# Performance work log

Hardware: AMD Instinct MI355X
Metric: run time of the kernel (lower is better)

The kernel has to match this reference:

```python
import jax, jax.numpy as jnp
import numpy as np

NEG_SLOPE = 0.2

def setup_inputs() -> dict:
    key = jax.random.key(0)
    ks = jax.random.split(key, 10)
    N, E, L, D, H = 100000, 3200000, 200000, 128, 128
    x = jax.random.normal(ks[0], (N, D), dtype=jnp.float32)
    edge_index = jax.random.randint(ks[1], (2, E), 0, N, dtype=jnp.int64)
    edge_label_index = jax.random.randint(ks[2], (2, L), 0, N, dtype=jnp.int64)
    s = 1.0 / np.sqrt(D)
    W1l = jax.random.uniform(ks[3], (D, H), minval=-s, maxval=s, dtype=jnp.float32)
    b1 = jax.random.uniform(ks[4], (H,), minval=-s, maxval=s, dtype=jnp.float32)
    W1r = jax.random.uniform(ks[5], (D, H), minval=-s, maxval=s, dtype=jnp.float32)
    s2 = 1.0 / np.sqrt(H)
    W2l = jax.random.uniform(ks[6], (H, H), minval=-s2, maxval=s2, dtype=jnp.float32)
    b2 = jax.random.uniform(ks[7], (H,), minval=-s2, maxval=s2, dtype=jnp.float32)
    W2r = jax.random.uniform(ks[8], (H, H), minval=-s2, maxval=s2, dtype=jnp.float32)
    return {"x": x, "edge_index": edge_index, "edge_label_index": edge_label_index,
            "W1l": W1l, "b1": b1, "W1r": W1r, "W2l": W2l, "b2": b2, "W2r": W2r}

def reference(x, edge_index, edge_label_index, W1l, b1, W1r, W2l, b2, W2r):
    N = x.shape[0]
    src, dst = edge_index[0], edge_index[1]
    # in-degree for mean aggregation (clamped to avoid div-by-zero, matching mean over empty = 0)
    deg = jax.ops.segment_sum(jnp.ones_like(dst, dtype=x.dtype), dst, num_segments=N)
    inv_deg = (1.0 / jnp.maximum(deg, 1.0))[:, None]

    def sage(h, Wl, b, Wr):
        # mean of source-node features over incoming edges at each target node
        agg = jax.ops.segment_sum(h[src], dst, num_segments=N) * inv_deg
        return agg @ Wl + b + h @ Wr

    h = sage(x, W1l, b1, W1r)
    h = jnp.where(h >= 0, h, NEG_SLOPE * h)  # leaky_relu; eval mode so no dropout
    h = sage(h, W2l, b2, W2r)
    x_src = h[edge_label_index[0]]
    x_trg = h[edge_label_index[1]]
    return jnp.sum(x_src * x_trg, axis=1)
```

## Files before the change

kernel.cpp:

```cpp
#include <hip/hip_runtime.h>
#include <hip/hip_fp16.h>


#define D128 128
#define BSHIFT 9
#define BNODES 512

typedef __bf16 bf16x8 __attribute__((ext_vector_type(8)));
typedef float  f32x4  __attribute__((ext_vector_type(4)));
typedef _Float16 h2   __attribute__((ext_vector_type(2)));

union uh2cast { unsigned u; h2 h; };
__device__ inline h2 uash2(unsigned u) { uh2cast c; c.u = u; return c.h; }

__device__ inline unsigned short f2bf(float f) {
    unsigned u = __float_as_uint(f);
    u = u + 0x7FFF + ((u >> 16) & 1);
    return (unsigned short)(u >> 16);
}
__device__ inline float bf2f(unsigned short s) {
    return __uint_as_float(((unsigned)s) << 16);
}
__device__ inline unsigned packbf2(float lo, float hi) {
    return (unsigned)f2bf(lo) | ((unsigned)f2bf(hi) << 16);
}
__device__ inline unsigned char f2e5(float f) {
    unsigned short h = __half_as_ushort(__float2half(f));
    h = (unsigned short)(h + 0x7F + ((h >> 8) & 1));
    return (unsigned char)(h >> 8);
}


__global__ void prep_kernel(const float* __restrict__ in, unsigned short* __restrict__ outb,
                            unsigned char* __restrict__ out8, int n4,
                            const float* __restrict__ W1l, const float* __restrict__ W1r,
                            const float* __restrict__ W2l, const float* __restrict__ W2r,
                            unsigned short* __restrict__ packed,
                            const int* __restrict__ dst, int* __restrict__ bh,
                            int E, int castBlocks, int histBlocks) {
    int bid = blockIdx.x;
    int t = threadIdx.x;
    if (bid < castBlocks) {
        int i = bid * 256 + t;
        if (i >= n4) return;
        float4 v = ((const float4*)in)[i];
        ushort4 ob;
        ob.x = f2bf(v.x); ob.y = f2bf(v.y); ob.z = f2bf(v.z); ob.w = f2bf(v.w);
        ((ushort4*)outb)[i] = ob;
        unsigned p = (unsigned)f2e5(v.x) | ((unsigned)f2e5(v.y) << 8) |
                     ((unsigned)f2e5(v.z) << 16) | ((unsigned)f2e5(v.w) << 24);
        ((unsigned*)out8)[i] = p;
    } else if (bid < castBlocks + 256) {
        int tid = (bid - castBlocks) * 256 + t;
        int layer = tid >> 15;
        int r = tid & 32767;
        int j    = r & 7;
        int lane = (r >> 3) & 63;
        int nt   = (r >> 9) & 7;
        int kc   = (r >> 12) & 7;
        int k   = kc * 32 + ((lane >> 4) << 3) + j;
        int col = nt * 16 + (lane & 15);
        const float* Wl = layer ? W2l : W1l;
        const float* Wr = layer ? W2r : W1r;
        float v = (k < 128) ? Wl[k * 128 + col] : Wr[(k - 128) * 128 + col];
        packed[tid] = f2bf(v);
    } else {
        __shared__ int h[256];
        int hb = bid - castBlocks - 256;
        if (hb >= histBlocks) return;
        h[t] = 0;
        __syncthreads();
        int base = hb * 8192;
#pragma unroll
        for (int k = 0; k < 32; ++k) {
            int e = base + k * 256 + t;
            if (e < E) atomicAdd(&h[dst[e] >> BSHIFT], 1);
        }
        __syncthreads();
        bh[hb * 256 + t] = h[t];
    }
}


__global__ void bucket_scan(const int* __restrict__ bh, int nhb,
                            int* __restrict__ bucket_base, int* __restrict__ bucket_cur,
                            int* __restrict__ rowptr, int NB, int N, int E) {
    __shared__ int sc[256];
    __shared__ int orig[256];
    int t = threadIdx.x;
    int v = 0;
    for (int b = 0; b < nhb; ++b) v += bh[b * 256 + t];
    if (t >= NB) v = 0;
    orig[t] = v;
    sc[t] = v;
    __syncthreads();
    for (int off = 1; off < 256; off <<= 1) {
        int a = (t >= off) ? sc[t - off] : 0;
        __syncthreads();
        sc[t] += a;
        __syncthreads();
    }
    int ex = sc[t] - orig[t];
    if (t < NB) { bucket_base[t] = ex; bucket_cur[t] = ex; }
    if (t == 0) { bucket_base[NB] = E; rowptr[N] = E; }
}

__global__ void scatter_kernel(const int* __restrict__ src, const int* __restrict__ dst,
                               int* __restrict__ bucket_cur, int* __restrict__ pairs,
                               int E, int NB) {
    __shared__ int hist[256], lscan[256], gbase[256];
    __shared__ int lsrc[1024], ldst[1024];
    int t = threadIdx.x;
    hist[t] = 0;
    __syncthreads();
    int base = blockIdx.x * 1024;
    int total = E - base; if (total > 1024) total = 1024;

    int ms[4], md[4], mb[4], mr[4];
#pragma unroll
    for (int k = 0; k < 4; ++k) {
        int i = k * 256 + t;
        int e = base + i;
        mb[k] = -1;
        if (i < total) {
            ms[k] = src[e];
            md[k] = dst[e];
            mb[k] = md[k] >> BSHIFT;
            mr[k] = atomicAdd(&hist[mb[k]], 1);
        }
    }
    __syncthreads();
    lscan[t] = hist[t];
    __syncthreads();
    for (int off = 1; off < 256; off <<= 1) {
        int a = (t >= off) ? lscan[t - off] : 0;
        __syncthreads();
        lscan[t] += a;
        __syncthreads();
    }
    lscan[t] -= hist[t];
    if (t < NB && hist[t] > 0) gbase[t] = atomicAdd(&bucket_cur[t], hist[t]);
    __syncthreads();
#pragma unroll
    for (int k = 0; k < 4; ++k) {
        if (mb[k] >= 0) {
            int idx = lscan[mb[k]] + mr[k];
            lsrc[idx] = ms[k];
            ldst[idx] = md[k];
        }
    }
    __syncthreads();
#pragma unroll
    for (int k = 0; k < 4; ++k) {
        int i = k * 256 + t;
        if (i < total) {
            int d = ldst[i];
            int b = d >> BSHIFT;
            int pos = gbase[b] + (i - lscan[b]);
            pairs[pos] = (lsrc[i] << BSHIFT) | (d & (BNODES - 1));
        }
    }
}

__global__ void bucket_fill(const int* __restrict__ pairs, const int* __restrict__ bucket_base,
                            int* __restrict__ rowptr, int* __restrict__ srcs, int N) {
    __shared__ int hist[BNODES], excl[BNODES], sc[BNODES];
    int b = blockIdx.x;
    int t = threadIdx.x;
    int node0 = b << BSHIFT;
    int pbeg = bucket_base[b];
    int pend = bucket_base[b + 1];
    hist[t] = 0;
    __syncthreads();
    for (int p = pbeg + t; p < pend; p += BNODES) {
        atomicAdd(&hist[pairs[p] & (BNODES - 1)], 1);
    }
    __syncthreads();
    sc[t] = hist[t];
    __syncthreads();
    for (int off = 1; off < BNODES; off <<= 1) {
        int a = (t >= off) ? sc[t - off] : 0;
        __syncthreads();
        sc[t] += a;
        __syncthreads();
    }
    excl[t] = sc[t] - hist[t];
    int node = node0 + t;
    if (node < N) rowptr[node] = pbeg + excl[t];
    __syncthreads();
    hist[t] = 0;
    __syncthreads();
    for (int p = pbeg + t; p < pend; p += BNODES) {
        int w = pairs[p];
        int dl = w & (BNODES - 1);
        int c = atomicAdd(&hist[dl], 1);
        srcs[pbeg + excl[dl] + c] = (int)(((unsigned)w) >> BSHIFT) << 4;
    }
}


__device__ inline void pkacc8(h2* A, uint2 v) {
    A[0] += uash2((v.x << 8) & 0xFF00FF00u);
    A[1] += uash2(v.x & 0xFF00FF00u);
    A[2] += uash2((v.y << 8) & 0xFF00FF00u);
    A[3] += uash2(v.y & 0xFF00FF00u);
}

__global__ void agg_kernel(const int* __restrict__ rowptr, const int* __restrict__ srcs,
                           const unsigned char* __restrict__ feat8,
                           unsigned short* __restrict__ out, int N) {
    int wave = threadIdx.x >> 6;
    int lane = threadIdx.x & 63;
    int q  = lane >> 4;
    int ql = lane & 15;
    int n = blockIdx.x * 4 + wave;
    if (n >= N) return;
    int beg = rowptr[n];
    int end = rowptr[n + 1];
    const uint2* f = (const uint2*)feat8;

    h2 A0[4], A1[4], A2[4], A3[4];
    h2 z; z[0] = (_Float16)0.f; z[1] = (_Float16)0.f;
#pragma unroll
    for (int k = 0; k < 4; ++k) { A0[k] = z; A1[k] = z; A2[k] = z; A3[k] = z; }

    int j = beg;
    int pre = (4 - (beg & 3)) & 3;
    if (pre > end - beg) pre = end - beg;
    if (q < pre) {
        uint2 v = f[srcs[j + q] + ql];
        pkacc8(A1, v);
    }
    j += pre;

    for (; j + 16 <= end; j += 16) {
        int4 e = *(const int4*)(srcs + j + 4 * q);
        uint2 v0 = f[e.x + ql];
        uint2 v1 = f[e.y + ql];
        uint2 v2 = f[e.z + ql];
        uint2 v3 = f[e.w + ql];
        pkacc8(A0, v0);
        pkacc8(A1, v1);
        pkacc8(A2, v2);
        pkacc8(A3, v3);
    }
    for (; j + 4 <= end; j += 4) {
        uint2 v = f[srcs[j + q] + ql];
        pkacc8(A0, v);
    }
    int rem = end - j;
    if (q < rem) {
        uint2 v = f[srcs[j + q] + ql];
        pkacc8(A2, v);
    }

    float c[8];
#pragma unroll
    for (int p = 0; p < 4; ++p) {
        float lo = (float)A0[p][0] + (float)A1[p][0] + (float)A2[p][0] + (float)A3[p][0];
        float hi = (float)A0[p][1] + (float)A1[p][1] + (float)A2[p][1] + (float)A3[p][1];
        int base = (p >> 1) * 4 + (p & 1);
        c[base] = lo;
        c[base + 2] = hi;
    }

#pragma unroll
    for (int k = 0; k < 8; ++k) {
        c[k] += __shfl_xor(c[k], 16, 64);
        c[k] += __shfl_xor(c[k], 32, 64);
    }

    int deg = end - beg;
    float inv = deg > 0 ? 1.0f / (float)deg : 0.f;
    if (q == 0) {
        uint4 r;
        r.x = packbf2(c[0] * inv, c[1] * inv);
        r.y = packbf2(c[2] * inv, c[3] * inv);
        r.z = packbf2(c[4] * inv, c[5] * inv);
        r.w = packbf2(c[6] * inv, c[7] * inv);
        ((uint4*)out)[(size_t)n * 16 + ql] = r;
    }
}


template <bool LEAKY>
__global__ void mm_kernel(const unsigned short* __restrict__ A,
                          const unsigned short* __restrict__ F,
                          const unsigned short* __restrict__ Wp,
                          const float* __restrict__ bias,
                          unsigned short* __restrict__ out,
                          unsigned char* __restrict__ out8, int N) {
    int wid = threadIdx.x >> 6;
    int lane = threadIdx.x & 63;
    int quad = lane >> 4;
    int m0 = (blockIdx.x * 4 + wid) * 32;

    int rowA0 = m0 + (lane & 15);
    int rowA1 = rowA0 + 16;
    if (rowA0 > N - 1) rowA0 = N - 1;
    if (rowA1 > N - 1) rowA1 = N - 1;

    f32x4 acc[2][8];
#pragma unroll
    for (int t = 0; t < 2; ++t)
#pragma unroll
        for (int nt = 0; nt < 8; ++nt) acc[t][nt] = (f32x4){0.f, 0.f, 0.f, 0.f};

#pragma unroll
    for (int kc = 0; kc < 8; ++kc) {
        const unsigned short* src = (kc < 4) ? (A + kc * 32) : (F + (kc - 4) * 32);
        bf16x8 af0 = *(const bf16x8*)(src + (size_t)rowA0 * D128 + quad * 8);
        bf16x8 af1 = *(const bf16x8*)(src + (size_t)rowA1 * D128 + quad * 8);
        const unsigned short* wp = Wp + ((size_t)kc * 8) * 512 + lane * 8;
#pragma unroll
        for (int nt = 0; nt < 8; ++nt) {
            bf16x8 bf = *(const bf16x8*)(wp + nt * 512);
            acc[0][nt] = __builtin_amdgcn_mfma_f32_16x16x32_bf16(af0, bf, acc[0][nt], 0, 0, 0);
            acc[1][nt] = __builtin_amdgcn_mfma_f32_16x16x32_bf16(af1, bf, acc[1][nt], 0, 0, 0);
        }
    }

#pragma unroll
    for (int nt = 0; nt < 8; ++nt) {
        int col = nt * 16 + (lane & 15);
        float bv = bias[col];
#pragma unroll
        for (int t = 0; t < 2; ++t) {
#pragma unroll
            for (int r = 0; r < 4; ++r) {
                int row = m0 + t * 16 + quad * 4 + r;
                if (row < N) {
                    float v = acc[t][nt][r] + bv;
                    if (LEAKY) v = v >= 0.f ? v : 0.2f * v;
                    out[(size_t)row * D128 + col] = f2bf(v);
                    if (out8) out8[(size_t)row * D128 + col] = f2e5(v);
                }
            }
        }
    }
}


__global__ void score_kernel(const int* __restrict__ eli, const unsigned short* __restrict__ h,
                             float* __restrict__ out, int L) {
    int wave = threadIdx.x >> 6;
    int lane = threadIdx.x & 63;
    int l0 = (blockIdx.x * 4 + wave) * 4;
    if (l0 >= L) return;
    const ushort2* h2p = (const ushort2*)h;
    int a[4], b[4];
#pragma unroll
    for (int k = 0; k < 4; ++k) {
        int l = l0 + k;
        if (l > L - 1) l = L - 1;
        a[k] = eli[l];
        b[k] = eli[L + l];
    }
    float p[4];
#pragma unroll
    for (int k = 0; k < 4; ++k) {
        ushort2 u = h2p[(size_t)a[k] * 64 + lane];
        ushort2 v = h2p[(size_t)b[k] * 64 + lane];
        p[k] = bf2f(u.x) * bf2f(v.x) + bf2f(u.y) * bf2f(v.y);
    }
#pragma unroll
    for (int off = 32; off > 0; off >>= 1) {
#pragma unroll
        for (int k = 0; k < 4; ++k) p[k] += __shfl_down(p[k], off, 64);
    }
    if (lane == 0) {
#pragma unroll
        for (int k = 0; k < 4; ++k) {
            if (l0 + k < L) out[l0 + k] = p[k];
        }
    }
}


extern "C" void kernel_launch(void* const* d_in, const int* in_sizes, int n_in,
                              void* d_out, int out_size, void* d_ws, size_t ws_size,
                              hipStream_t stream) {
    const float* x   = (const float*)d_in[0];
    const int*   ei  = (const int*)d_in[1];
    const int*   eli = (const int*)d_in[2];
    const float* W1l = (const float*)d_in[3];
    const float* b1  = (const float*)d_in[4];
    const float* W1r = (const float*)d_in[5];
    const float* W2l = (const float*)d_in[6];
    const float* b2  = (const float*)d_in[7];
    const float* W2r = (const float*)d_in[8];

    const int N = in_sizes[0] / D128;
    const int E = in_sizes[1] / 2;
    const int L = in_sizes[2] / 2;
    const int* srcp = ei;
    const int* dstp = ei + E;
    const int NB = (N + BNODES - 1) >> BSHIFT;

    char* ws = (char*)d_ws;
    size_t off = 0;
    auto alloc = [&](size_t bytes) -> void* {
        void* p = ws + off;
        off += (bytes + 255) & ~(size_t)255;
        return p;
    };
    const int histBlocks = (E + 8191) / 8192;
    int*   rowptr = (int*)alloc((size_t)(N + 1) * sizeof(int));
    int*   bh     = (int*)alloc((size_t)histBlocks * 256 * sizeof(int));
    int*   bbase  = (int*)alloc(257 * sizeof(int));
    int*   bcur   = (int*)alloc(256 * sizeof(int));
    int*   pairs  = (int*)alloc((size_t)E * sizeof(int));
    int*   srcs   = (int*)alloc(((size_t)E + 16) * sizeof(int));
    unsigned short* xb   = (unsigned short*)alloc((size_t)N * D128 * 2);
    unsigned char*  x8   = (unsigned char*)alloc((size_t)N * D128);
    unsigned char*  h1f8 = (unsigned char*)alloc((size_t)N * D128);
    unsigned short* aggb = (unsigned short*)alloc((size_t)N * D128 * 2);
    unsigned short* h1b  = (unsigned short*)alloc((size_t)N * D128 * 2);
    unsigned short* h2b  = (unsigned short*)alloc((size_t)N * D128 * 2);
    unsigned short* Wp   = (unsigned short*)alloc(2 * 32768 * 2);
    (void)ws_size; (void)n_in; (void)out_size;

    int n4 = N * D128 / 4;
    int castBlocks = (n4 + 255) / 256;
    prep_kernel<<<castBlocks + 256 + histBlocks, 256, 0, stream>>>(
        x, xb, x8, n4, W1l, W1r, W2l, W2r, Wp, dstp, bh, E, castBlocks, histBlocks);

    bucket_scan<<<1, 256, 0, stream>>>(bh, histBlocks, bbase, bcur, rowptr, NB, N, E);
    scatter_kernel<<<(E + 1023) / 1024, 256, 0, stream>>>(srcp, dstp, bcur, pairs, E, NB);
    bucket_fill<<<NB, BNODES, 0, stream>>>(pairs, bbase, rowptr, srcs, N);

    agg_kernel<<<(N + 3) / 4, 256, 0, stream>>>(rowptr, srcs, x8, aggb, N);
    mm_kernel<true><<<(N + 127) / 128, 256, 0, stream>>>(aggb, xb, Wp, b1, h1b, h1f8, N);

    agg_kernel<<<(N + 3) / 4, 256, 0, stream>>>(rowptr, srcs, h1f8, aggb, N);
    mm_kernel<false><<<(N + 127) / 128, 256, 0, stream>>>(aggb, h1b, Wp + 32768, b2, h2b,
                                                          (unsigned char*)nullptr, N);

    score_kernel<<<(L + 15) / 16, 256, 0, stream>>>(eli, h2b, (float*)d_out, L);
}
```

Before: 510.9 us.

## Fuse neighbor aggregation with MFMA projection via LDS staging per wave

Merges the separate aggregation and matmul kernels into one kernel. Each wave aggregates 16 nodes sequentially into LDS, then runs the 16-row MFMA projection directly from LDS, so the intermediate aggregated bf16 buffer is never written to or read back from global memory. Each wave now handles its 16 nodes one at a time instead of one node per wave, which lowers gather parallelism and latency hiding and may cause load imbalance. Also uses a hardware bf8 convert builtin when available and unrolls the bucket histogram reduction.

```diff
diff --git a/kernel.cpp b/kernel.cpp
--- a/kernel.cpp
+++ b/kernel.cpp
@@ -25,9 +25,13 @@
     return (unsigned)f2bf(lo) | ((unsigned)f2bf(hi) << 16);
 }
 __device__ inline unsigned char f2e5(float f) {
+#if __has_builtin(__builtin_amdgcn_cvt_pk_bf8_f32)
+    return (unsigned char)(__builtin_amdgcn_cvt_pk_bf8_f32(f, f, 0, false) & 0xFF);
+#else
     unsigned short h = __half_as_ushort(__float2half(f));
     h = (unsigned short)(h + 0x7F + ((h >> 8) & 1));
     return (unsigned char)(h >> 8);
+#endif
 }
 
 
@@ -88,8 +92,20 @@
     __shared__ int sc[256];
     __shared__ int orig[256];
     int t = threadIdx.x;
-    int v = 0;
-    for (int b = 0; b < nhb; ++b) v += bh[b * 256 + t];
+    int a0 = 0, a1 = 0, a2 = 0, a3 = 0, a4 = 0, a5 = 0, a6 = 0, a7 = 0;
+    int b = 0;
+    for (; b + 8 <= nhb; b += 8) {
+        a0 += bh[(b + 0) * 256 + t];
+        a1 += bh[(b + 1) * 256 + t];
+        a2 += bh[(b + 2) * 256 + t];
+        a3 += bh[(b + 3) * 256 + t];
+        a4 += bh[(b + 4) * 256 + t];
+        a5 += bh[(b + 5) * 256 + t];
+        a6 += bh[(b + 6) * 256 + t];
+        a7 += bh[(b + 7) * 256 + t];
+    }
+    for (; b < nhb; ++b) a0 += bh[b * 256 + t];
+    int v = ((a0 + a1) + (a2 + a3)) + ((a4 + a5) + (a6 + a7));
     if (t >= NB) v = 0;
     orig[t] = v;
     sc[t] = v;
@@ -206,135 +222,119 @@
     A[3] += uash2(v.y & 0xFF00FF00u);
 }
 
-__global__ void agg_kernel(const int* __restrict__ rowptr, const int* __restrict__ srcs,
-                           const unsigned char* __restrict__ feat8,
-                           unsigned short* __restrict__ out, int N) {
-    int wave = threadIdx.x >> 6;
+template <bool LEAKY>
+__global__ void aggmm_kernel(const int* __restrict__ rowptr, const int* __restrict__ srcs,
+                             const unsigned char* __restrict__ feat8,
+                             const unsigned short* __restrict__ F,
+                             const unsigned short* __restrict__ Wp,
+                             const float* __restrict__ bias,
+                             unsigned short* __restrict__ out,
+                             unsigned char* __restrict__ out8, int N) {
+    __shared__ unsigned short ldsA[4 * 16 * D128];
+    int wid = threadIdx.x >> 6;
     int lane = threadIdx.x & 63;
     int q  = lane >> 4;
     int ql = lane & 15;
-    int n = blockIdx.x * 4 + wave;
-    if (n >= N) return;
-    int beg = rowptr[n];
-    int end = rowptr[n + 1];
+    int m0 = (blockIdx.x * 4 + wid) * 16;
     const uint2* f = (const uint2*)feat8;
 
-    h2 A0[4], A1[4], A2[4], A3[4];
-    h2 z; z[0] = (_Float16)0.f; z[1] = (_Float16)0.f;
-#pragma unroll
-    for (int k = 0; k < 4; ++k) { A0[k] = z; A1[k] = z; A2[k] = z; A3[k] = z; }
-
-    int j = beg;
-    int pre = (4 - (beg & 3)) & 3;
-    if (pre > end - beg) pre = end - beg;
-    if (q < pre) {
-        uint2 v = f[srcs[j + q] + ql];
-        pkacc8(A1, v);
-    }
-    j += pre;
-
-    for (; j + 16 <= end; j += 16) {
-        int4 e = *(const int4*)(srcs + j + 4 * q);
-        uint2 v0 = f[e.x + ql];
-        uint2 v1 = f[e.y + ql];
-        uint2 v2 = f[e.z + ql];
-        uint2 v3 = f[e.w + ql];
-        pkacc8(A0, v0);
-        pkacc8(A1, v1);
-        pkacc8(A2, v2);
-        pkacc8(A3, v3);
-    }
-    for (; j + 4 <= end; j += 4) {
-        uint2 v = f[srcs[j + q] + ql];
-        pkacc8(A0, v);
-    }
-    int rem = end - j;
-    if (q < rem) {
-        uint2 v = f[srcs[j + q] + ql];
-        pkacc8(A2, v);
-    }
-
-    float c[8];
-#pragma unroll
-    for (int p = 0; p < 4; ++p) {
-        float lo = (float)A0[p][0] + (float)A1[p][0] + (float)A2[p][0] + (float)A3[p][0];
-        float hi = (float)A0[p][1] + (float)A1[p][1] + (float)A2[p][1] + (float)A3[p][1];
-        int base = (p >> 1) * 4 + (p & 1);
-        c[base] = lo;
-        c[base + 2] = hi;
-    }
-
-#pragma unroll
-    for (int k = 0; k < 8; ++k) {
-        c[k] += __shfl_xor(c[k], 16, 64);
-        c[k] += __shfl_xor(c[k], 32, 64);
-    }
-
-    int deg = end - beg;
-    float inv = deg > 0 ? 1.0f / (float)deg : 0.f;
-    if (q == 0) {
-        uint4 r;
-        r.x = packbf2(c[0] * inv, c[1] * inv);
-        r.y = packbf2(c[2] * inv, c[3] * inv);
-        r.z = packbf2(c[4] * inv, c[5] * inv);
-        r.w = packbf2(c[6] * inv, c[7] * inv);
-        ((uint4*)out)[(size_t)n * 16 + ql] = r;
-    }
-}
-
-
-template <bool LEAKY>
-__global__ void mm_kernel(const unsigned short* __restrict__ A,
-                          const unsigned short* __restrict__ F,
-                          const unsigned short* __restrict__ Wp,
-                          const float* __restrict__ bias,
-                          unsigned short* __restrict__ out,
-                          unsigned char* __restrict__ out8, int N) {
-    int wid = threadIdx.x >> 6;
-    int lane = threadIdx.x & 63;
-    int quad = lane >> 4;
-    int m0 = (blockIdx.x * 4 + wid) * 32;
-
-    int rowA0 = m0 + (lane & 15);
-    int rowA1 = rowA0 + 16;
-    if (rowA0 > N - 1) rowA0 = N - 1;
-    if (rowA1 > N - 1) rowA1 = N - 1;
-
-    f32x4 acc[2][8];
-#pragma unroll
-    for (int t = 0; t < 2; ++t)
-#pragma unroll
-        for (int nt = 0; nt < 8; ++nt) acc[t][nt] = (f32x4){0.f, 0.f, 0.f, 0.f};
+    for (int r = 0; r < 16; ++r) {
+        int n = m0 + r;
+        if (n >= N) break;
+        int beg = rowptr[n];
+        int end = rowptr[n + 1];
+
+        h2 A0[4], A1[4], A2[4], A3[4];
+        h2 z; z[0] = (_Float16)0.f; z[1] = (_Float16)0.f;
+#pragma unroll
+        for (int k = 0; k < 4; ++k) { A0[k] = z; A1[k] = z; A2[k] = z; A3[k] = z; }
+
+        int j = beg;
+        for (; j + 16 <= end; j += 16) {
+            int e0 = srcs[j + q];
+            int e1 = srcs[j + 4 + q];
+            int e2 = srcs[j + 8 + q];
+            int e3 = srcs[j + 12 + q];
+            uint2 v0 = f[e0 + ql];
+            uint2 v1 = f[e1 + ql];
+            uint2 v2 = f[e2 + ql];
+            uint2 v3 = f[e3 + ql];
+            pkacc8(A0, v0);
+            pkacc8(A1, v1);
+            pkacc8(A2, v2);
+            pkacc8(A3, v3);
+        }
+        for (; j + 4 <= end; j += 4) {
+            uint2 v = f[srcs[j + q] + ql];
+            pkacc8(A0, v);
+        }
+        int rem = end - j;
+        if (q < rem) {
+            uint2 v = f[srcs[j + q] + ql];
+            pkacc8(A1, v);
+        }
+
+        float c[8];
+#pragma unroll
+        for (int p = 0; p < 4; ++p) {
+            float lo = (float)A0[p][0] + (float)A1[p][0] + (float)A2[p][0] + (float)A3[p][0];
+            float hi = (float)A0[p][1] + (float)A1[p][1] + (float)A2[p][1] + (float)A3[p][1];
+            int base = (p >> 1) * 4 + (p & 1);
+            c[base] = lo;
+            c[base + 2] = hi;
+        }
+#pragma unroll
+        for (int k = 0; k < 8; ++k) {
+            c[k] += __shfl_xor(c[k], 16, 64);
+            c[k] += __shfl_xor(c[k], 32, 64);
+        }
+        int deg = end - beg;
+        float inv = deg > 0 ? 1.0f / (float)deg : 0.f;
+        if (q == 0) {
+            uint4 rr;
+            rr.x = packbf2(c[0] * inv, c[1] * inv);
+            rr.y = packbf2(c[2] * inv, c[3] * inv);
+            rr.z = packbf2(c[4] * inv, c[5] * inv);
+            rr.w = packbf2(c[6] * inv, c[7] * inv);
+            ((uint4*)ldsA)[wid * 256 + r * 16 + ql] = rr;
+        }
+    }
+    __syncthreads();
+
+    int rl = lane & 15;
+    int rowF = m0 + rl;
+    if (rowF > N - 1) rowF = N - 1;
+    const unsigned short* ldsW = ldsA + wid * 16 * D128;
+
+    f32x4 acc[8];
+#pragma unroll
+    for (int nt = 0; nt < 8; ++nt) acc[nt] = (f32x4){0.f, 0.f, 0.f, 0.f};
 
 #pragma unroll
     for (int kc = 0; kc < 8; ++kc) {
-        const unsigned short* src = (kc < 4) ? (A + kc * 32) : (F + (kc - 4) * 32);
-        bf16x8 af0 = *(const bf16x8*)(src + (size_t)rowA0 * D128 + quad * 8);
-        bf16x8 af1 = *(const bf16x8*)(src + (size_t)rowA1 * D128 + quad * 8);
+        bf16x8 af;
+        if (kc < 4) af = *(const bf16x8*)(ldsW + rl * D128 + kc * 32 + q * 8);
+        else        af = *(const bf16x8*)(F + (size_t)rowF * D128 + (kc - 4) * 32 + q * 8);
         const unsigned short* wp = Wp + ((size_t)kc * 8) * 512 + lane * 8;
 #pragma unroll
         for (int nt = 0; nt < 8; ++nt) {
             bf16x8 bf = *(const bf16x8*)(wp + nt * 512);
-            acc[0][nt] = __builtin_amdgcn_mfma_f32_16x16x32_bf16(af0, bf, acc[0][nt], 0, 0, 0);
-            acc[1][nt] = __builtin_amdgcn_mfma_f32_16x16x32_bf16(af1, bf, acc[1][nt], 0, 0, 0);
+            acc[nt] = __builtin_amdgcn_mfma_f32_16x16x32_bf16(af, bf, acc[nt], 0, 0, 0);
         }
     }
 
 #pragma unroll
     for (int nt = 0; nt < 8; ++nt) {
-        int col = nt * 16 + (lane & 15);
+        int col = nt * 16 + rl;
         float bv = bias[col];
 #pragma unroll
-        for (int t = 0; t < 2; ++t) {
-#pragma unroll
-            for (int r = 0; r < 4; ++r) {
-                int row = m0 + t * 16 + quad * 4 + r;
-                if (row < N) {
-                    float v = acc[t][nt][r] + bv;
-                    if (LEAKY) v = v >= 0.f ? v : 0.2f * v;
-                    out[(size_t)row * D128 + col] = f2bf(v);
-                    if (out8) out8[(size_t)row * D128 + col] = f2e5(v);
-                }
+        for (int r = 0; r < 4; ++r) {
+            int row = m0 + q * 4 + r;
+            if (row < N) {
+                float v = acc[nt][r] + bv;
+                if (LEAKY) v = v >= 0.f ? v : 0.2f * v;
+                out[(size_t)row * D128 + col] = f2bf(v);
+                if (out8) out8[(size_t)row * D128 + col] = f2e5(v);
             }
         }
     }
@@ -414,7 +414,6 @@
     unsigned short* xb   = (unsigned short*)alloc((size_t)N * D128 * 2);
     unsigned char*  x8   = (unsigned char*)alloc((size_t)N * D128);
     unsigned char*  h1f8 = (unsigned char*)alloc((size_t)N * D128);
-    unsigned short* aggb = (unsigned short*)alloc((size_t)N * D128 * 2);
     unsigned short* h1b  = (unsigned short*)alloc((size_t)N * D128 * 2);
     unsigned short* h2b  = (unsigned short*)alloc((size_t)N * D128 * 2);
     unsigned short* Wp   = (unsigned short*)alloc(2 * 32768 * 2);
@@ -429,12 +428,12 @@
     scatter_kernel<<<(E + 1023) / 1024, 256, 0, stream>>>(srcp, dstp, bcur, pairs, E, NB);
     bucket_fill<<<NB, BNODES, 0, stream>>>(pairs, bbase, rowptr, srcs, N);
 
-    agg_kernel<<<(N + 3) / 4, 256, 0, stream>>>(rowptr, srcs, x8, aggb, N);
-    mm_kernel<true><<<(N + 127) / 128, 256, 0, stream>>>(aggb, xb, Wp, b1, h1b, h1f8, N);
-
-    agg_kernel<<<(N + 3) / 4, 256, 0, stream>>>(rowptr, srcs, h1f8, aggb, N);
-    mm_kernel<false><<<(N + 127) / 128, 256, 0, stream>>>(aggb, h1b, Wp + 32768, b2, h2b,
-                                                          (unsigned char*)nullptr, N);
+    int mmBlocks = (N + 63) / 64;
+    aggmm_kernel<true><<<mmBlocks, 256, 0, stream>>>(rowptr, srcs, x8, xb, Wp, b1,
+                                                     h1b, h1f8, N);
+
+    aggmm_kernel<false><<<mmBlocks, 256, 0, stream>>>(rowptr, srcs, h1f8, h1b, Wp + 32768,
+                                                      b2, h2b, (unsigned char*)nullptr, N);
 
     score_kernel<<<(L + 15) / 16, 256, 0, stream>>>(eli, h2b, (float*)d_out, L);
 }
```

After: 454.5 us. 11.0% less time.
